# Optimization experiments

Hardware: AMD Instinct MI355X
Metric: run time of the kernel (lower is better)

The kernel has to match this reference:

```python
import jax, jax.numpy as jnp
import numpy as np

N_RAYS = 4096
NUM_STEPS = 768
MIN_NEAR_LIDAR = 0.01
LIDAR_MAX_DEPTH = 0.81
BOUND = 1.0
DENSITY_SCALE = 1.0
HID = 64
OUT_DIM = 2  # out_lidar_color_dim (intensity + raydrop)


def setup_inputs() -> dict:
    key = jax.random.key(0)
    ks = jax.random.split(key, 12)
    rays_o = jax.random.normal(ks[0], (N_RAYS, 3), jnp.float32) * 0.1
    rd = jax.random.normal(ks[1], (N_RAYS, 3), jnp.float32)
    rays_d = rd / jnp.linalg.norm(rd, axis=-1, keepdims=True)
    time = jax.random.uniform(ks[2], (N_RAYS, 1), jnp.float32)
    s = lambda fan: 1.0 / np.sqrt(fan)
    W1 = jax.random.normal(ks[3], (4, HID), jnp.float32) * s(4)
    b1 = jnp.zeros((HID,), jnp.float32)
    W2 = jax.random.normal(ks[4], (HID, HID), jnp.float32) * s(HID)
    b2 = jnp.zeros((HID,), jnp.float32)
    w_sig = jax.random.normal(ks[5], (HID, 1), jnp.float32) * s(HID)
    b_sig = jnp.zeros((1,), jnp.float32)
    Wc1 = jax.random.normal(ks[6], (3 + HID, HID), jnp.float32) * s(3 + HID)
    bc1 = jnp.zeros((HID,), jnp.float32)
    Wc2 = jax.random.normal(ks[7], (HID, OUT_DIM), jnp.float32) * s(HID)
    bc2 = jnp.zeros((OUT_DIM,), jnp.float32)
    return {"rays_o": rays_o, "rays_d": rays_d, "time": time,
            "W1": W1, "b1": b1, "W2": W2, "b2": b2,
            "w_sig": w_sig, "b_sig": b_sig,
            "Wc1": Wc1, "bc1": bc1, "Wc2": Wc2, "bc2": bc2}


def reference(rays_o, rays_d, time, W1, b1, W2, b2, w_sig, b_sig, Wc1, bc1, Wc2, bc2):
    N, S = rays_o.shape[0], NUM_STEPS
    nears = MIN_NEAR_LIDAR
    fars = LIDAR_MAX_DEPTH
    # stratified z values along each ray (no perturb)
    z = jnp.linspace(0.0, 1.0, S, dtype=rays_o.dtype)          # [S]
    z_vals = jnp.broadcast_to(nears + (fars - nears) * z, (N, S))
    sample_dist = (fars - nears) / S
    # sample points, clamped to AABB [-bound, bound]^3
    xyzs = rays_o[:, None, :] + rays_d[:, None, :] * z_vals[..., None]  # [N,S,3]
    xyzs = jnp.clip(xyzs, -BOUND, BOUND)
    # surrogate time-conditioned density field (NVSF 4D field)
    t = jnp.broadcast_to(time[:, None, :], (N, S, 1))
    h = jax.nn.relu(jnp.concatenate([xyzs, t], -1) @ W1 + b1)  # [N,S,HID]
    h = jax.nn.relu(h @ W2 + b2)
    sigma = jax.nn.softplus(h @ w_sig + b_sig)[..., 0]          # [N,S]
    # surrogate lidar color head (dir + geo features)
    dirs = jnp.broadcast_to(rays_d[:, None, :], (N, S, 3))
    c = jax.nn.relu(jnp.concatenate([dirs, h], -1) @ Wc1 + bc1)
    rgbs = jax.nn.sigmoid(c @ Wc2 + bc2)                        # [N,S,OUT_DIM]
    # alpha compositing
    deltas = z_vals[..., 1:] - z_vals[..., :-1]
    deltas = jnp.concatenate([deltas, jnp.full_like(deltas[..., :1], sample_dist)], -1)
    alphas = 1.0 - jnp.exp(-deltas * DENSITY_SCALE * sigma)     # [N,S]
    alphas_shifted = jnp.concatenate(
        [jnp.ones_like(alphas[..., :1]), 1.0 - alphas + 1e-15], -1)
    weights = alphas * jnp.cumprod(alphas_shifted, axis=-1)[..., :-1]
    weights_sum = jnp.sum(weights, axis=-1)                     # [N]
    depth = jnp.sum(weights * z_vals, axis=-1)                  # [N]
    image = jnp.sum(weights[..., None] * rgbs, axis=-2)         # [N,OUT_DIM]
    # lidar branch: no background compositing
    return depth, image, weights_sum, weights, z_vals
```

## Files before the change

kernel.cpp:

```cpp
#include <hip/hip_runtime.h>
#include <hip/hip_bf16.h>
#include <math.h>

#define NR 4096
#define NS 768

#define OFF_IMAGE   (NR)
#define OFF_WSUM    (NR*3)
#define OFF_WEIGHTS (NR*4)
#define OFF_ZVALS   (NR*4 + NR*NS)

typedef short bf16x8 __attribute__((ext_vector_type(8)));
typedef float f32x4  __attribute__((ext_vector_type(4)));

static __device__ __forceinline__ unsigned cvt_pk_bf16(float a, float b){
    unsigned r;
    asm("v_cvt_pk_bf16_f32 %0, %1, %2" : "=v"(r) : "v"(a), "v"(b));
    return r;
}
static __device__ __forceinline__ f32x4 zero4(){ f32x4 r = {0.f,0.f,0.f,0.f}; return r; }

__global__ __launch_bounds__(256, 2) void mlp_mfma_kernel(
    const float* __restrict__ rays_o, const float* __restrict__ rays_d,
    const float* __restrict__ timev,
    const float* __restrict__ W1, const float* __restrict__ b1,
    const float* __restrict__ W2, const float* __restrict__ b2,
    const float* __restrict__ w_sig, const float* __restrict__ b_sig,
    const float* __restrict__ Wc1, const float* __restrict__ bc1,
    const float* __restrict__ Wc2, const float* __restrict__ bc2,
    float* __restrict__ alpha_out,
    float* __restrict__ rgb_out)
{
    __shared__ __align__(16) unsigned bounce[4][2048];
    __shared__ __align__(16) unsigned stash[16*64*4];
    const int wid  = threadIdx.x >> 6;
    const int lane = threadIdx.x & 63;
    const int g = lane >> 4;
    const int c = lane & 15;

    if (wid == 0) {
        #pragma unroll
        for (int ft = 0; ft < 4; ++ft) {
            const int col = ft*16 + c;
            unsigned u0=0,u1=0,u2=0,u3=0, d0=0,d1=0;
            if (g == 0) {
                u0 = cvt_pk_bf16(W1[0*64+col], W1[1*64+col]);
                u1 = cvt_pk_bf16(W1[2*64+col], W1[3*64+col]);
                u2 = cvt_pk_bf16(b1[col], 0.f);
                d0 = cvt_pk_bf16(Wc1[0*64+col], Wc1[1*64+col]);
                d1 = cvt_pk_bf16(Wc1[2*64+col], bc1[col]);
            }
            unsigned* p = &stash[(ft*64 + lane)*4];
            p[0]=u0; p[1]=u1; p[2]=u2; p[3]=u3;
            unsigned* q = &stash[((4+ft)*64 + lane)*4];
            q[0]=d0; q[1]=d1; q[2]=0; q[3]=0;
        }
        #pragma unroll
        for (int kt = 0; kt < 2; ++kt) {
            unsigned s[4], w[4];
            #pragma unroll
            for (int p = 0; p < 4; ++p) {
                int k = kt*32 + 8*g + 2*p;
                s[p] = (c == 0) ? cvt_pk_bf16(w_sig[k], w_sig[k+1]) : 0u;
                w[p] = (c < 2)  ? cvt_pk_bf16(Wc2[k*2+c], Wc2[(k+1)*2+c]) : 0u;
            }
            unsigned* ps = &stash[((8+kt)*64 + lane)*4];
            ps[0]=s[0]; ps[1]=s[1]; ps[2]=s[2]; ps[3]=s[3];
            unsigned* pw = &stash[((10+kt)*64 + lane)*4];
            pw[0]=w[0]; pw[1]=w[1]; pw[2]=w[2]; pw[3]=w[3];
        }
        #pragma unroll
        for (int ft = 0; ft < 4; ++ft) {
            float* pb = reinterpret_cast<float*>(&stash[((12+ft)*64 + lane)*4]);
            #pragma unroll
            for (int r = 0; r < 4; ++r) pb[r] = b2[ft*16 + g*4 + r];
        }
    }

    auto ldfrag = [&](const float* __restrict__ W, int k0, int col)->bf16x8 {
        union { bf16x8 v; unsigned u[4]; } r;
        #pragma unroll
        for (int p = 0; p < 4; ++p) {
            int k = k0 + 2*p;
            r.u[p] = cvt_pk_bf16(W[k*64 + col], W[(k+1)*64 + col]);
        }
        return r.v;
    };
    bf16x8 bW2A[2][4], bWc1A[2][4];
    #pragma unroll
    for (int ft = 0; ft < 4; ++ft) {
        const int col = ft*16 + c;
        #pragma unroll
        for (int kt = 0; kt < 2; ++kt) {
            bW2A[kt][ft]  = ldfrag(W2,         kt*32 + 8*g, col);
            bWc1A[kt][ft] = ldfrag(Wc1 + 3*64, kt*32 + 8*g, col);
        }
    }
    const float bsg = b_sig[0];
    f32x4 bc2v;
    bc2v[0] = (g==0) ? bc2[0] : 0.f;
    bc2v[1] = (g==0) ? bc2[1] : 0.f;
    bc2v[2] = 0.f; bc2v[3] = 0.f;

    __syncthreads();

    unsigned* BW = &bounce[wid][0];
    const int wbase = c*8 + g*2;
    const int rbase = (g>>1)*128 + c*8 + (g&1)*4;
    auto SL = [&](int s)->bf16x8 {
        return *reinterpret_cast<const bf16x8*>(&stash[(s*64 + lane)*4]);
    };
    auto RD = [&](int kt, int nt)->bf16x8 {
        return *reinterpret_cast<const bf16x8*>(&BW[rbase + (nt*4 + kt*2)*128]);
    };

    const int gwave = blockIdx.x*4 + wid;

    #pragma unroll 1
    for (int tt = 0; tt < 6; ++tt) {
        const int tile = gwave*6 + tt;
        const int n  = tile / 12;
        const int s0 = (tile - n*12) * 64;
        const int s  = s0 + lane;

        const float z  = 0.01f + 0.8f * ((float)s * (1.0f/767.0f));
        const float ox = rays_o[3*n+0], oy = rays_o[3*n+1], oz = rays_o[3*n+2];
        const float dx = rays_d[3*n+0], dy = rays_d[3*n+1], dz = rays_d[3*n+2];
        const float tm = timev[n];

        const float px = fminf(fmaxf(fmaf(dx, z, ox), -1.f), 1.f);
        const float py = fminf(fmaxf(fmaf(dy, z, oy), -1.f), 1.f);
        const float pz = fminf(fmaxf(fmaf(dz, z, oz), -1.f), 1.f);
        const unsigned p01 = cvt_pk_bf16(px, py);
        const unsigned p23 = cvt_pk_bf16(pz, tm);

        f32x4 acc[4][4];

        {
            bf16x8 a1[4];
            #pragma unroll
            for (int ft = 0; ft < 4; ++ft) a1[ft] = SL(ft);
            #pragma unroll
            for (int nt = 0; nt < 4; ++nt) {
                unsigned q0 = (unsigned)__shfl((int)p01, nt*16 + c);
                unsigned q1 = (unsigned)__shfl((int)p23, nt*16 + c);
                union { bf16x8 v; unsigned u[4]; } b;
                b.u[0] = (g==0) ? q0 : 0u;
                b.u[1] = (g==0) ? q1 : 0u;
                b.u[2] = (g==0) ? 0x00003F80u : 0u;
                b.u[3] = 0u;
                #pragma unroll
                for (int ft = 0; ft < 4; ++ft)
                    acc[ft][nt] = __builtin_amdgcn_mfma_f32_16x16x32_bf16(
                        a1[ft], b.v, zero4(), 0, 0, 0);
            }
        }
        #pragma unroll
        for (int ft = 0; ft < 4; ++ft)
            #pragma unroll
            for (int nt = 0; nt < 4; ++nt) {
                unsigned pk0 = cvt_pk_bf16(fmaxf(acc[ft][nt][0],0.f), fmaxf(acc[ft][nt][1],0.f));
                unsigned pk1 = cvt_pk_bf16(fmaxf(acc[ft][nt][2],0.f), fmaxf(acc[ft][nt][3],0.f));
                *reinterpret_cast<uint2*>(&BW[wbase + (nt*4+ft)*128]) = make_uint2(pk0, pk1);
            }

        {
            f32x4 b2v[4];
            #pragma unroll
            for (int ft = 0; ft < 4; ++ft)
                b2v[ft] = *reinterpret_cast<const f32x4*>(&stash[((12+ft)*64 + lane)*4]);
            #pragma unroll
            for (int nt = 0; nt < 4; ++nt) {
                bf16x8 f0 = RD(0, nt), f1 = RD(1, nt);
                #pragma unroll
                for (int ft = 0; ft < 4; ++ft) {
                    f32x4 d = __builtin_amdgcn_mfma_f32_16x16x32_bf16(bW2A[0][ft], f0, b2v[ft], 0,0,0);
                    acc[ft][nt] = __builtin_amdgcn_mfma_f32_16x16x32_bf16(bW2A[1][ft], f1, d, 0,0,0);
                }
            }
        }
        #pragma unroll
        for (int ft = 0; ft < 4; ++ft)
            #pragma unroll
            for (int nt = 0; nt < 4; ++nt) {
                unsigned pk0 = cvt_pk_bf16(fmaxf(acc[ft][nt][0],0.f), fmaxf(acc[ft][nt][1],0.f));
                unsigned pk1 = cvt_pk_bf16(fmaxf(acc[ft][nt][2],0.f), fmaxf(acc[ft][nt][3],0.f));
                *reinterpret_cast<uint2*>(&BW[wbase + (nt*4+ft)*128]) = make_uint2(pk0, pk1);
            }

        f32x4 sigD[4];
        {
            bf16x8 ad[4];
            #pragma unroll
            for (int ft = 0; ft < 4; ++ft) ad[ft] = SL(4+ft);
            bf16x8 ws0 = SL(8), ws1 = SL(9);
            union { bf16x8 v; unsigned u[4]; } fd;
            fd.u[0] = (g==0) ? cvt_pk_bf16(dx, dy) : 0u;
            fd.u[1] = (g==0) ? cvt_pk_bf16(dz, 1.0f) : 0u;
            fd.u[2] = 0u; fd.u[3] = 0u;
            #pragma unroll
            for (int nt = 0; nt < 4; ++nt) {
                bf16x8 f0 = RD(0, nt), f1 = RD(1, nt);
                #pragma unroll
                for (int ft = 0; ft < 4; ++ft) {
                    f32x4 d = __builtin_amdgcn_mfma_f32_16x16x32_bf16(bWc1A[0][ft], f0, zero4(), 0,0,0);
                    d = __builtin_amdgcn_mfma_f32_16x16x32_bf16(bWc1A[1][ft], f1, d, 0,0,0);
                    acc[ft][nt] = __builtin_amdgcn_mfma_f32_16x16x32_bf16(ad[ft], fd.v, d, 0,0,0);
                }
                f32x4 sd = __builtin_amdgcn_mfma_f32_16x16x32_bf16(ws0, f0, zero4(), 0,0,0);
                sigD[nt] = __builtin_amdgcn_mfma_f32_16x16x32_bf16(ws1, f1, sd, 0,0,0);
            }
        }
        #pragma unroll
        for (int ft = 0; ft < 4; ++ft)
            #pragma unroll
            for (int nt = 0; nt < 4; ++nt) {
                unsigned pk0 = cvt_pk_bf16(fmaxf(acc[ft][nt][0],0.f), fmaxf(acc[ft][nt][1],0.f));
                unsigned pk1 = cvt_pk_bf16(fmaxf(acc[ft][nt][2],0.f), fmaxf(acc[ft][nt][3],0.f));
                *reinterpret_cast<uint2*>(&BW[wbase + (nt*4+ft)*128]) = make_uint2(pk0, pk1);
            }

        {
            float v0 = __shfl(sigD[0][0], c);
            float v1 = __shfl(sigD[1][0], c);
            float v2 = __shfl(sigD[2][0], c);
            float v3 = __shfl(sigD[3][0], c);
            float pre = (g==0) ? v0 : ((g==1) ? v1 : ((g==2) ? v2 : v3));
            pre += bsg;
            float sig = fmaxf(pre, 0.f) + __logf(1.f + __expf(-fabsf(pre)));
            float dl  = (s == NS-1) ? (0.8f/768.0f) : (0.8f/767.0f);
            alpha_out[tile*64 + lane] = 1.0f - __expf(-dl * sig);
        }

        {
            bf16x8 c20 = SL(10), c21 = SL(11);
            f32x4 rgbD[4];
            #pragma unroll
            for (int nt = 0; nt < 4; ++nt) {
                bf16x8 f0 = RD(0, nt), f1 = RD(1, nt);
                f32x4 d = __builtin_amdgcn_mfma_f32_16x16x32_bf16(c20, f0, bc2v, 0,0,0);
                rgbD[nt] = __builtin_amdgcn_mfma_f32_16x16x32_bf16(c21, f1, d, 0,0,0);
            }
            float a0 = __shfl(rgbD[0][0], c), b0 = __shfl(rgbD[0][1], c);
            float a1 = __shfl(rgbD[1][0], c), b1v_ = __shfl(rgbD[1][1], c);
            float a2 = __shfl(rgbD[2][0], c), b2_ = __shfl(rgbD[2][1], c);
            float a3 = __shfl(rgbD[3][0], c), b3 = __shfl(rgbD[3][1], c);
            float r0 = (g==0) ? a0 : ((g==1) ? a1 : ((g==2) ? a2 : a3));
            float r1 = (g==0) ? b0 : ((g==1) ? b1v_ : ((g==2) ? b2_ : b3));
            r0 = 1.0f / (1.0f + __expf(-r0));
            r1 = 1.0f / (1.0f + __expf(-r1));
            *reinterpret_cast<float2*>(&rgb_out[2*(tile*64 + lane)]) = make_float2(r0, r1);
        }
    }
}

__global__ __launch_bounds__(256) void composite_kernel(
    const float* __restrict__ rgb,
    float* __restrict__ out)
{
    int gtid = blockIdx.x * 256 + threadIdx.x;
    int ray  = gtid >> 6;
    int lane = threadIdx.x & 63;
    if (ray >= NR) return;

    float* __restrict__ depth_o = out;
    float* __restrict__ image_o = out + OFF_IMAGE;
    float* __restrict__ wsum_o  = out + OFF_WSUM;
    float* __restrict__ w_o     = out + OFF_WEIGHTS;
    float* __restrict__ z_o     = out + OFF_ZVALS;

    float T = 1.0f;
    float depth = 0.0f, wsum = 0.0f, im0 = 0.0f, im1 = 0.0f;

    for (int ch = 0; ch < NS/64; ++ch) {
        int s   = ch*64 + lane;
        int idx = ray*NS + s;
        float a  = w_o[idx];
        float zv = 0.01f + 0.8f * ((float)s * (1.0f/767.0f));
        float f  = 1.0f - a + 1e-15f;

        float p = f;
        #pragma unroll
        for (int off = 1; off < 64; off <<= 1) {
            float v = __shfl_up(p, off, 64);
            if (lane >= off) p *= v;
        }
        float excl = __shfl_up(p, 1, 64);
        if (lane == 0) excl = 1.0f;

        float wgt = a * T * excl;

        float r0 = rgb[2*idx + 0], r1 = rgb[2*idx + 1];
        depth = fmaf(wgt, zv, depth);
        wsum += wgt;
        im0   = fmaf(wgt, r0, im0);
        im1   = fmaf(wgt, r1, im1);

        w_o[idx] = wgt;
        z_o[idx] = zv;

        T *= __shfl(p, 63, 64);
    }

    #pragma unroll
    for (int off = 32; off >= 1; off >>= 1) {
        depth += __shfl_down(depth, off, 64);
        wsum  += __shfl_down(wsum , off, 64);
        im0   += __shfl_down(im0  , off, 64);
        im1   += __shfl_down(im1  , off, 64);
    }
    if (lane == 0) {
        depth_o[ray]      = depth;
        image_o[2*ray+0]  = im0;
        image_o[2*ray+1]  = im1;
        wsum_o[ray]       = wsum;
    }
}

extern "C" void kernel_launch(void* const* d_in, const int* in_sizes, int n_in,
                              void* d_out, int out_size, void* d_ws, size_t ws_size,
                              hipStream_t stream) {
    const float* rays_o = (const float*)d_in[0];
    const float* rays_d = (const float*)d_in[1];
    const float* timev  = (const float*)d_in[2];
    const float* W1     = (const float*)d_in[3];
    const float* b1     = (const float*)d_in[4];
    const float* W2     = (const float*)d_in[5];
    const float* b2     = (const float*)d_in[6];
    const float* w_sig  = (const float*)d_in[7];
    const float* b_sig  = (const float*)d_in[8];
    const float* Wc1    = (const float*)d_in[9];
    const float* bc1    = (const float*)d_in[10];
    const float* Wc2    = (const float*)d_in[11];
    const float* bc2    = (const float*)d_in[12];

    float* out   = (float*)d_out;
    float* alpha = out + OFF_WEIGHTS;
    float* rgb   = (float*)d_ws;

    dim3 blk(256);
    hipLaunchKernelGGL(mlp_mfma_kernel, dim3(2048), blk, 0, stream,
                       rays_o, rays_d, timev, W1, b1, W2, b2, w_sig, b_sig,
                       Wc1, bc1, Wc2, bc2, alpha, rgb);

    hipLaunchKernelGGL(composite_kernel, dim3((NR*64)/256), blk, 0, stream, rgb, out);
}
```

Measured before the change: 123.2 us.

## Process MLP tiles in 16-sample slices to cut registers and LDS, raise occupancy

Restructures the per-wave MLP loop so each 64-sample tile is handled as four 16-sample slices through all layers, instead of keeping all four column tiles of accumulators live. This shrinks the live accumulator set and the per-wave LDS bounce buffer by four times. It raises the occupancy hint from 2 to 3 blocks per SM and rebalances the grid to 3072 blocks with 4 tiles per wave. The cost is less MFMA instruction-level parallelism within a wave and more serialized LDS round trips per slice, and weight fragments are reloaded from LDS per slice. It relies on compiler-only fences instead of explicit waits for intra-wave LDS ordering.

New measurement: 144.3 us. 17.2% more time.

```diff
diff --git a/kernel.cpp b/kernel.cpp
--- a/kernel.cpp
+++ b/kernel.cpp
@@ -19,8 +19,9 @@
     return r;
 }
 static __device__ __forceinline__ f32x4 zero4(){ f32x4 r = {0.f,0.f,0.f,0.f}; return r; }
-
-__global__ __launch_bounds__(256, 2) void mlp_mfma_kernel(
+static __device__ __forceinline__ void ldsfence(){ asm volatile("" ::: "memory"); }
+
+__global__ __launch_bounds__(256, 3) void mlp_mfma_kernel(
     const float* __restrict__ rays_o, const float* __restrict__ rays_d,
     const float* __restrict__ timev,
     const float* __restrict__ W1, const float* __restrict__ b1,
@@ -31,7 +32,7 @@
     float* __restrict__ alpha_out,
     float* __restrict__ rgb_out)
 {
-    __shared__ __align__(16) unsigned bounce[4][2048];
+    __shared__ __align__(16) unsigned bounce[4][512];
     __shared__ __align__(16) unsigned stash[16*64*4];
     const int wid  = threadIdx.x >> 6;
     const int lane = threadIdx.x & 63;
@@ -110,15 +111,17 @@
     auto SL = [&](int s)->bf16x8 {
         return *reinterpret_cast<const bf16x8*>(&stash[(s*64 + lane)*4]);
     };
-    auto RD = [&](int kt, int nt)->bf16x8 {
-        return *reinterpret_cast<const bf16x8*>(&BW[rbase + (nt*4 + kt*2)*128]);
+    auto BOUNCE = [&](const f32x4& a, int ft){
+        unsigned pk0 = cvt_pk_bf16(fmaxf(a[0],0.f), fmaxf(a[1],0.f));
+        unsigned pk1 = cvt_pk_bf16(fmaxf(a[2],0.f), fmaxf(a[3],0.f));
+        *reinterpret_cast<uint2*>(&BW[wbase + ft*128]) = make_uint2(pk0, pk1);
     };
 
     const int gwave = blockIdx.x*4 + wid;
 
     #pragma unroll 1
-    for (int tt = 0; tt < 6; ++tt) {
-        const int tile = gwave*6 + tt;
+    for (int tt = 0; tt < 4; ++tt) {
+        const int tile = gwave*4 + tt;
         const int n  = tile / 12;
         const int s0 = (tile - n*12) * 64;
         const int s  = s0 + lane;
@@ -134,16 +137,20 @@
         const unsigned p01 = cvt_pk_bf16(px, py);
         const unsigned p23 = cvt_pk_bf16(pz, tm);
 
-        f32x4 acc[4][4];
-
-        {
-            bf16x8 a1[4];
-            #pragma unroll
-            for (int ft = 0; ft < 4; ++ft) a1[ft] = SL(ft);
-            #pragma unroll
-            for (int nt = 0; nt < 4; ++nt) {
-                unsigned q0 = (unsigned)__shfl((int)p01, nt*16 + c);
-                unsigned q1 = (unsigned)__shfl((int)p23, nt*16 + c);
+        union { bf16x8 v; unsigned u[4]; } fd;
+        fd.u[0] = (g==0) ? cvt_pk_bf16(dx, dy) : 0u;
+        fd.u[1] = (g==0) ? cvt_pk_bf16(dz, 1.0f) : 0u;
+        fd.u[2] = 0u; fd.u[3] = 0u;
+
+        float sg[4], rg0[4], rg1[4];
+
+        #pragma unroll
+        for (int sl = 0; sl < 4; ++sl) {
+            f32x4 acc[4];
+
+            {
+                unsigned q0 = (unsigned)__shfl((int)p01, sl*16 + c);
+                unsigned q1 = (unsigned)__shfl((int)p23, sl*16 + c);
                 union { bf16x8 v; unsigned u[4]; } b;
                 b.u[0] = (g==0) ? q0 : 0u;
                 b.u[1] = (g==0) ? q1 : 0u;
@@ -151,100 +158,76 @@
                 b.u[3] = 0u;
                 #pragma unroll
                 for (int ft = 0; ft < 4; ++ft)
-                    acc[ft][nt] = __builtin_amdgcn_mfma_f32_16x16x32_bf16(
-                        a1[ft], b.v, zero4(), 0, 0, 0);
-            }
-        }
-        #pragma unroll
-        for (int ft = 0; ft < 4; ++ft)
-            #pragma unroll
-            for (int nt = 0; nt < 4; ++nt) {
-                unsigned pk0 = cvt_pk_bf16(fmaxf(acc[ft][nt][0],0.f), fmaxf(acc[ft][nt][1],0.f));
-                unsigned pk1 = cvt_pk_bf16(fmaxf(acc[ft][nt][2],0.f), fmaxf(acc[ft][nt][3],0.f));
-                *reinterpret_cast<uint2*>(&BW[wbase + (nt*4+ft)*128]) = make_uint2(pk0, pk1);
-            }
-
-        {
-            f32x4 b2v[4];
-            #pragma unroll
-            for (int ft = 0; ft < 4; ++ft)
-                b2v[ft] = *reinterpret_cast<const f32x4*>(&stash[((12+ft)*64 + lane)*4]);
-            #pragma unroll
-            for (int nt = 0; nt < 4; ++nt) {
-                bf16x8 f0 = RD(0, nt), f1 = RD(1, nt);
+                    acc[ft] = __builtin_amdgcn_mfma_f32_16x16x32_bf16(
+                        SL(ft), b.v, zero4(), 0, 0, 0);
+            }
+            ldsfence();
+            #pragma unroll
+            for (int ft = 0; ft < 4; ++ft) BOUNCE(acc[ft], ft);
+            ldsfence();
+
+            {
+                bf16x8 f0 = *reinterpret_cast<const bf16x8*>(&BW[rbase]);
+                bf16x8 f1 = *reinterpret_cast<const bf16x8*>(&BW[rbase + 256]);
+                ldsfence();
                 #pragma unroll
                 for (int ft = 0; ft < 4; ++ft) {
-                    f32x4 d = __builtin_amdgcn_mfma_f32_16x16x32_bf16(bW2A[0][ft], f0, b2v[ft], 0,0,0);
-                    acc[ft][nt] = __builtin_amdgcn_mfma_f32_16x16x32_bf16(bW2A[1][ft], f1, d, 0,0,0);
+                    f32x4 b2v = *reinterpret_cast<const f32x4*>(&stash[((12+ft)*64 + lane)*4]);
+                    f32x4 d = __builtin_amdgcn_mfma_f32_16x16x32_bf16(bW2A[0][ft], f0, b2v, 0,0,0);
+                    acc[ft]  = __builtin_amdgcn_mfma_f32_16x16x32_bf16(bW2A[1][ft], f1, d, 0,0,0);
                 }
             }
-        }
-        #pragma unroll
-        for (int ft = 0; ft < 4; ++ft)
-            #pragma unroll
-            for (int nt = 0; nt < 4; ++nt) {
-                unsigned pk0 = cvt_pk_bf16(fmaxf(acc[ft][nt][0],0.f), fmaxf(acc[ft][nt][1],0.f));
-                unsigned pk1 = cvt_pk_bf16(fmaxf(acc[ft][nt][2],0.f), fmaxf(acc[ft][nt][3],0.f));
-                *reinterpret_cast<uint2*>(&BW[wbase + (nt*4+ft)*128]) = make_uint2(pk0, pk1);
-            }
-
-        f32x4 sigD[4];
-        {
-            bf16x8 ad[4];
-            #pragma unroll
-            for (int ft = 0; ft < 4; ++ft) ad[ft] = SL(4+ft);
-            bf16x8 ws0 = SL(8), ws1 = SL(9);
-            union { bf16x8 v; unsigned u[4]; } fd;
-            fd.u[0] = (g==0) ? cvt_pk_bf16(dx, dy) : 0u;
-            fd.u[1] = (g==0) ? cvt_pk_bf16(dz, 1.0f) : 0u;
-            fd.u[2] = 0u; fd.u[3] = 0u;
-            #pragma unroll
-            for (int nt = 0; nt < 4; ++nt) {
-                bf16x8 f0 = RD(0, nt), f1 = RD(1, nt);
+            ldsfence();
+            #pragma unroll
+            for (int ft = 0; ft < 4; ++ft) BOUNCE(acc[ft], ft);
+            ldsfence();
+
+            {
+                bf16x8 f0 = *reinterpret_cast<const bf16x8*>(&BW[rbase]);
+                bf16x8 f1 = *reinterpret_cast<const bf16x8*>(&BW[rbase + 256]);
+                ldsfence();
                 #pragma unroll
                 for (int ft = 0; ft < 4; ++ft) {
                     f32x4 d = __builtin_amdgcn_mfma_f32_16x16x32_bf16(bWc1A[0][ft], f0, zero4(), 0,0,0);
                     d = __builtin_amdgcn_mfma_f32_16x16x32_bf16(bWc1A[1][ft], f1, d, 0,0,0);
-                    acc[ft][nt] = __builtin_amdgcn_mfma_f32_16x16x32_bf16(ad[ft], fd.v, d, 0,0,0);
+                    acc[ft] = __builtin_amdgcn_mfma_f32_16x16x32_bf16(SL(4+ft), fd.v, d, 0,0,0);
                 }
-                f32x4 sd = __builtin_amdgcn_mfma_f32_16x16x32_bf16(ws0, f0, zero4(), 0,0,0);
-                sigD[nt] = __builtin_amdgcn_mfma_f32_16x16x32_bf16(ws1, f1, sd, 0,0,0);
-            }
-        }
-        #pragma unroll
-        for (int ft = 0; ft < 4; ++ft)
-            #pragma unroll
-            for (int nt = 0; nt < 4; ++nt) {
-                unsigned pk0 = cvt_pk_bf16(fmaxf(acc[ft][nt][0],0.f), fmaxf(acc[ft][nt][1],0.f));
-                unsigned pk1 = cvt_pk_bf16(fmaxf(acc[ft][nt][2],0.f), fmaxf(acc[ft][nt][3],0.f));
-                *reinterpret_cast<uint2*>(&BW[wbase + (nt*4+ft)*128]) = make_uint2(pk0, pk1);
-            }
+                f32x4 sd = __builtin_amdgcn_mfma_f32_16x16x32_bf16(SL(8), f0, zero4(), 0,0,0);
+                sd = __builtin_amdgcn_mfma_f32_16x16x32_bf16(SL(9), f1, sd, 0,0,0);
+                sg[sl] = sd[0];
+            }
+            ldsfence();
+            #pragma unroll
+            for (int ft = 0; ft < 4; ++ft) BOUNCE(acc[ft], ft);
+            ldsfence();
+
+            {
+                bf16x8 f0 = *reinterpret_cast<const bf16x8*>(&BW[rbase]);
+                bf16x8 f1 = *reinterpret_cast<const bf16x8*>(&BW[rbase + 256]);
+                ldsfence();
+                f32x4 d = __builtin_amdgcn_mfma_f32_16x16x32_bf16(SL(10), f0, bc2v, 0,0,0);
+                d = __builtin_amdgcn_mfma_f32_16x16x32_bf16(SL(11), f1, d, 0,0,0);
+                rg0[sl] = d[0];
+                rg1[sl] = d[1];
+            }
+        }
 
         {
-            float v0 = __shfl(sigD[0][0], c);
-            float v1 = __shfl(sigD[1][0], c);
-            float v2 = __shfl(sigD[2][0], c);
-            float v3 = __shfl(sigD[3][0], c);
+            float v0 = __shfl(sg[0], c);
+            float v1 = __shfl(sg[1], c);
+            float v2 = __shfl(sg[2], c);
+            float v3 = __shfl(sg[3], c);
             float pre = (g==0) ? v0 : ((g==1) ? v1 : ((g==2) ? v2 : v3));
             pre += bsg;
             float sig = fmaxf(pre, 0.f) + __logf(1.f + __expf(-fabsf(pre)));
             float dl  = (s == NS-1) ? (0.8f/768.0f) : (0.8f/767.0f);
             alpha_out[tile*64 + lane] = 1.0f - __expf(-dl * sig);
         }
-
         {
-            bf16x8 c20 = SL(10), c21 = SL(11);
-            f32x4 rgbD[4];
-            #pragma unroll
-            for (int nt = 0; nt < 4; ++nt) {
-                bf16x8 f0 = RD(0, nt), f1 = RD(1, nt);
-                f32x4 d = __builtin_amdgcn_mfma_f32_16x16x32_bf16(c20, f0, bc2v, 0,0,0);
-                rgbD[nt] = __builtin_amdgcn_mfma_f32_16x16x32_bf16(c21, f1, d, 0,0,0);
-            }
-            float a0 = __shfl(rgbD[0][0], c), b0 = __shfl(rgbD[0][1], c);
-            float a1 = __shfl(rgbD[1][0], c), b1v_ = __shfl(rgbD[1][1], c);
-            float a2 = __shfl(rgbD[2][0], c), b2_ = __shfl(rgbD[2][1], c);
-            float a3 = __shfl(rgbD[3][0], c), b3 = __shfl(rgbD[3][1], c);
+            float a0 = __shfl(rg0[0], c), b0 = __shfl(rg1[0], c);
+            float a1 = __shfl(rg0[1], c), b1v_ = __shfl(rg1[1], c);
+            float a2 = __shfl(rg0[2], c), b2_ = __shfl(rg1[2], c);
+            float a3 = __shfl(rg0[3], c), b3 = __shfl(rg1[3], c);
             float r0 = (g==0) ? a0 : ((g==1) ? a1 : ((g==2) ? a2 : a3));
             float r1 = (g==0) ? b0 : ((g==1) ? b1v_ : ((g==2) ? b2_ : b3));
             r0 = 1.0f / (1.0f + __expf(-r0));
@@ -339,7 +322,7 @@
     float* rgb   = (float*)d_ws;
 
     dim3 blk(256);
-    hipLaunchKernelGGL(mlp_mfma_kernel, dim3(2048), blk, 0, stream,
+    hipLaunchKernelGGL(mlp_mfma_kernel, dim3(3072), blk, 0, stream,
                        rays_o, rays_d, timev, W1, b1, W2, b2, w_sig, b_sig,
                        Wc1, bc1, Wc2, bc2, alpha, rgb);
 
```
